# Kernel tuning notes

Hardware: AMD Instinct MI355X
Metric: run time of the kernel (lower is better)

Reference implementation:

```python
import jax, jax.numpy as jnp
from jax import lax
import numpy as np

N, I, O = 64, 8, 8
B = 512
S_EX, S_PHI, S_RHO = 10, 60, 60  # S_phi must equal S_rho (alpha loops feed S_rho-sized h into the GRUs)
N_ACTIONS, N_ROLES = 5, 7


def _gru(x, h, Wih, Whh, bih, bhh):
    # torch.nn.GRUCell math
    gi = x @ Wih.T + bih
    gh = h @ Whh.T + bhh
    ir, iz, inn = jnp.split(gi, 3, axis=-1)
    hr, hz, hn = jnp.split(gh, 3, axis=-1)
    r = jax.nn.sigmoid(ir + hr)
    zg = jax.nn.sigmoid(iz + hz)
    n = jnp.tanh(inn + r * hn)
    return (1.0 - zg) * n + zg * h


def setup_inputs() -> dict:
    key = jax.random.key(0)
    ks = jax.random.split(key, 24)
    f32 = jnp.float32
    z = jax.random.normal(ks[0], (B, N, S_EX), f32)
    dz = jax.random.normal(ks[1], (B, N, S_EX), f32)
    has = (jax.random.uniform(ks[2], (B, N)) < 0.9).astype(f32)
    adj = (jnp.triu(jax.random.uniform(ks[3], (N, N)), 1) > 0.7).astype(jnp.int32)

    def lin(k, o, i):
        return (jax.random.normal(k, (o, i), f32) * np.float32(1.0 / np.sqrt(i)))

    d = dict(z=z, dz=dz, has=has, adj=adj)
    d['Wih_f'] = lin(ks[4], 3 * S_PHI, S_RHO)
    d['Whh_f'] = lin(ks[5], 3 * S_PHI, S_PHI)
    d['bih_f'] = jax.random.normal(ks[6], (3 * S_PHI,), f32) * 0.02
    d['bhh_f'] = jax.random.normal(ks[7], (3 * S_PHI,), f32) * 0.02
    d['Wih_b'] = lin(ks[8], 3 * S_PHI, S_RHO)
    d['Whh_b'] = lin(ks[9], 3 * S_PHI, S_PHI)
    d['bih_b'] = jax.random.normal(ks[10], (3 * S_PHI,), f32) * 0.02
    d['bhh_b'] = jax.random.normal(ks[11], (3 * S_PHI,), f32) * 0.02
    d['Wf'] = lin(ks[12], S_RHO, S_PHI + 2 * S_EX)
    d['bf'] = jax.random.normal(ks[13], (S_RHO,), f32) * 0.02
    d['Wb'] = lin(ks[14], S_RHO, S_PHI + 2 * S_EX)
    d['bb'] = jax.random.normal(ks[15], (S_RHO,), f32) * 0.02
    d['Wa'] = lin(ks[16], N_ACTIONS, 2 * S_PHI)
    d['ba'] = jax.random.normal(ks[17], (N_ACTIONS,), f32) * 0.02
    d['Wc'] = lin(ks[18], 1, 2 * S_PHI)
    d['bc'] = jax.random.normal(ks[19], (1,), f32) * 0.02
    d['Wu'] = lin(ks[20], N_ROLES, 2 * S_RHO)
    d['bu'] = jax.random.normal(ks[21], (N_ROLES,), f32) * 0.02
    return d


def reference(z, dz, has, adj,
              Wih_f, Whh_f, bih_f, bhh_f,
              Wih_b, Whh_b, bih_b, bhh_b,
              Wf, bf, Wb, bb, Wa, ba, Wc, bc, Wu, bu):
    Bn, Nn = has.shape
    dt = z.dtype
    adjf = adj.astype(dt)

    # ---- forward sweep over nodes in ascending order ----
    def fwd_outer(rho, i):
        def inner(h, j):
            hn = _gru(rho[j], h, Wih_f, Whh_f, bih_f, bhh_f)
            blend = adjf[j, i] * has[:, j][:, None]  # edge exists AND source node present
            return h + blend * (hn - h), None
        h, _ = lax.scan(inner, jnp.zeros((Bn, S_PHI), dt), jnp.arange(Nn))
        rho_i = jnp.tanh(jnp.concatenate([h, z[:, i], dz[:, i]], 1) @ Wf.T + bf)
        return rho.at[i].set(rho_i), None

    rho_f, _ = lax.scan(fwd_outer, jnp.zeros((Nn, Bn, S_RHO), dt), jnp.arange(Nn))

    # ---- backward sweep over nodes in descending order ----
    def bwd_outer(rho, i):
        def inner(h, j):
            hn = _gru(rho[j], h, Wih_b, Whh_b, bih_b, bhh_b)
            blend = adjf[i, j] * has[:, j][:, None]  # out-edges of i, visited descending
            return h + blend * (hn - h), None
        h, _ = lax.scan(inner, jnp.zeros((Bn, S_PHI), dt), jnp.arange(Nn - 1, -1, -1))
        rho_i = jnp.concatenate([h, z[:, i], dz[:, i]], 1) @ Wb.T + bb
        return rho.at[i].set(rho_i), None

    rho_b, _ = lax.scan(bwd_outer, jnp.zeros((Nn, Bn, S_RHO), dt), jnp.arange(Nn - 1, -1, -1))

    # ---- aggregate outputs (last O nodes) and inputs (first I nodes) ----
    h = jnp.zeros((Bn, S_RHO), dt)
    for i in range(N - O, N):
        hn = _gru(rho_f[i], h, Wih_f, Whh_f, bih_f, bhh_f)
        h = h + has[:, i][:, None] * (hn - h)
    alpha_f = h
    h = jnp.zeros((Bn, S_RHO), dt)
    for i in reversed(range(I)):
        hn = _gru(rho_b[i], h, Wih_b, Whh_b, bih_b, bhh_b)
        h = h + has[:, i][:, None] * (hn - h)
    alpha_b = h

    ab = jnp.concatenate([alpha_f, alpha_b], 1)
    omega = ab @ Wa.T + ba          # [B, 5]
    value = ab @ Wc.T + bc          # [B, 1]

    feats = jnp.concatenate([rho_f, rho_b], -1)           # [N, B, 2*S_rho]
    psi = jnp.einsum('nbs,rs->brn', feats, Wu) + bu[None, :, None]  # [B, 7, N]
    m = has[:, None, :]
    psi = -60.0 * (1.0 - m) + psi * m  # interpolate(-60, psi, has)

    instr_prob = jax.nn.softmax(omega, axis=1)
    role_prob = jax.nn.softmax(psi, axis=2)
    return instr_prob, role_prob, value
```

## Files before the change

kernel.cpp:

```cpp
#include <hip/hip_runtime.h>
#include <hip/hip_bf16.h>

#define NN 64
#define BATCH 512
#define SP 60
#define SG 180
#define SEX 10
#define CATD 80
#define NA 5
#define NR 7
#define OO 8
#define II 8

typedef unsigned long long u64;
typedef unsigned short u16;
typedef unsigned int u32;
typedef unsigned char u8;

#define OFF_Z     0
#define OFF_DZ    327680
#define OFF_HAS   655360
#define OFF_WIHF  688128
#define OFF_WHHF  698928
#define OFF_BIHF  709728
#define OFF_BHHF  709908
#define OFF_WIHB  710088
#define OFF_WHHB  720888
#define OFF_BIHB  731688
#define OFF_BHHB  731868
#define OFF_WF    732048
#define OFF_BF    736848
#define OFF_WB    736908
#define OFF_BB    741708
#define OFF_WA    741768
#define OFF_BA    742368
#define OFF_WC    742373
#define OFF_BC    742493
#define OFF_WU    742494
#define OFF_BU    743334
#define CONV_TOTAL 743341
#define OFF_FLAG  743342
#define OFF_RHOF  743344
#define OFF_RHOB  (OFF_RHOF + 1966080)
#define OFF_ALF   (OFF_RHOB + 1966080)
#define OFF_ALB   (OFF_ALF + 30720)
#define OUT_TOTAL 232448

typedef _Float16 f16;
typedef _Float16 half2_t __attribute__((ext_vector_type(2)));
typedef _Float16 f16x8 __attribute__((ext_vector_type(8)));
typedef float f32x4 __attribute__((ext_vector_type(4)));

__device__ __forceinline__ float us2f(u16 v){
  return __uint_as_float(((u32)v) << 16);
}
__device__ __forceinline__ u16 f2bf(float f){
  __hip_bfloat16 h = __float2bfloat16(f);
  return *reinterpret_cast<u16*>(&h);
}
__device__ __forceinline__ float rcp_(float x){ return __builtin_amdgcn_rcpf(x); }
__device__ __forceinline__ float sigm(float x){
  return rcp_(1.f + __expf(-x));
}
__device__ __forceinline__ float tanh_(float x){
  float e = __expf(2.f*fabsf(x));
  float t = 1.f - 2.f*rcp_(e + 1.f);
  return copysignf(t, x);
}
__device__ __forceinline__ u32 pack2(float a, float b){
  half2_t h; h[0] = (f16)a; h[1] = (f16)b;
  return __builtin_bit_cast(u32, h);
}
__device__ __forceinline__ float fdot2_(u32 a, u32 b, float c){
  return __builtin_amdgcn_fdot2(__builtin_bit_cast(half2_t, a),
                                __builtin_bit_cast(half2_t, b), c, false);
}
__device__ __forceinline__ f16x8 bc16(uint4 v){ return __builtin_bit_cast(f16x8, v); }
__device__ __forceinline__ f32x4 mfma16(f16x8 a, f16x8 b, f32x4 c){
  return __builtin_amdgcn_mfma_f32_16x16x32_f16(a, b, c, 0, 0, 0);
}

struct HP { uint4 q[8]; };
__device__ __forceinline__ u32 hpc(const HP& p, int k){
  const uint4& v = p.q[k>>2];
  switch(k&3){ case 0: return v.x; case 1: return v.y; case 2: return v.z; default: return v.w; }
}

__device__ __forceinline__ int detect_bf16(const u32* w){
  int f = 0;
  for (int i=0;i<256;i++) f |= (w[i] == 0x3F803F80u) ? 1 : 0;
  return f;
}

__global__ __launch_bounds__(256) void conv_in(
  const void* z, const void* dz, const void* has,
  const void* WihF, const void* WhhF, const void* bihF, const void* bhhF,
  const void* WihB, const void* WhhB, const void* bihB, const void* bhhB,
  const void* Wf_, const void* bf_, const void* Wb_, const void* bb_,
  const void* Wa, const void* ba, const void* Wc, const void* bc,
  const void* Wu, const void* bu, float* ws)
{
  const int isbf = detect_bf16((const u32*)has);
  if (blockIdx.x == 0 && threadIdx.x == 0) ws[OFF_FLAG] = (float)isbf;
  int idx = blockIdx.x*256 + threadIdx.x;
  if (idx >= CONV_TOTAL) return;
  const void* src; int loc;
  if      (idx < OFF_DZ  ){ src=z;    loc=idx-OFF_Z;    }
  else if (idx < OFF_HAS ){ src=dz;   loc=idx-OFF_DZ;   }
  else if (idx < OFF_WIHF){ src=has;  loc=idx-OFF_HAS;  }
  else if (idx < OFF_WHHF){ src=WihF; loc=idx-OFF_WIHF; }
  else if (idx < OFF_BIHF){ src=WhhF; loc=idx-OFF_WHHF; }
  else if (idx < OFF_BHHF){ src=bihF; loc=idx-OFF_BIHF; }
  else if (idx < OFF_WIHB){ src=bhhF; loc=idx-OFF_BHHF; }
  else if (idx < OFF_WHHB){ src=WihB; loc=idx-OFF_WIHB; }
  else if (idx < OFF_BIHB){ src=WhhB; loc=idx-OFF_WHHB; }
  else if (idx < OFF_BHHB){ src=bihB; loc=idx-OFF_BIHB; }
  else if (idx < OFF_WF  ){ src=bhhB; loc=idx-OFF_BHHB; }
  else if (idx < OFF_BF  ){ src=Wf_;  loc=idx-OFF_WF;   }
  else if (idx < OFF_WB  ){ src=bf_;  loc=idx-OFF_BF;   }
  else if (idx < OFF_BB  ){ src=Wb_;  loc=idx-OFF_WB;   }
  else if (idx < OFF_WA  ){ src=bb_;  loc=idx-OFF_BB;   }
  else if (idx < OFF_BA  ){ src=Wa;   loc=idx-OFF_WA;   }
  else if (idx < OFF_WC  ){ src=ba;   loc=idx-OFF_BA;   }
  else if (idx < OFF_BC  ){ src=Wc;   loc=idx-OFF_WC;   }
  else if (idx < OFF_WU  ){ src=bc;   loc=idx-OFF_BC;   }
  else if (idx < OFF_BU  ){ src=Wu;   loc=idx-OFF_WU;   }
  else                    { src=bu;   loc=idx-OFF_BU;   }
  float v = isbf ? us2f(((const u16*)src)[loc]) : ((const float*)src)[loc];
  ws[idx] = v;
}

__global__ __launch_bounds__(64, 1) void dir_kernel(const int* __restrict__ adj,
                                                    float* __restrict__ ws)
{
  const int u   = threadIdx.x;
  const int ml  = u & 15;
  const int q   = u >> 4;
  const int bid = blockIdx.x;
  const int bwd = bid >> 9;
  const int b   = bid & 511;

  const float* Wih  = ws + (bwd ? OFF_WIHB : OFF_WIHF);
  const float* Whh  = ws + (bwd ? OFF_WHHB : OFF_WHHF);
  const float* bih  = ws + (bwd ? OFF_BIHB : OFF_BIHF);
  const float* bhh  = ws + (bwd ? OFF_BHHB : OFF_BHHF);
  const float* Wcat = ws + (bwd ? OFF_WB   : OFF_WF);
  const float* bcat = ws + (bwd ? OFF_BB   : OFF_BF);
  const float* zc   = ws + OFF_Z;
  const float* dzc  = ws + OFF_DZ;
  const float* hasc = ws + OFF_HAS;
  float* rho   = ws + (bwd ? OFF_RHOB : OFF_RHOF);
  float* alpha = ws + (bwd ? OFF_ALB  : OFF_ALF);

  __shared__ uint4 sH4[65][9];
  __shared__ uint4 sRhoPad[8];
  __shared__ uint4 sRhoHist[8][8];
  __shared__ float sRhoOut[NN][SP];
  __shared__ u32 sZp[NN][5];
  __shared__ u32 sDZp[NN][5];
  __shared__ float sHas[NN];
  __shared__ u64 sRowM[NN];
  __shared__ u8 sConsL[NN][64];
  __shared__ int sConsCnt[NN];

  #define ROWB(I) ((char*)&sH4[(I)][0])
  const u32 BIASW = 0x3C000000u;

  u64 rowm = 0;
  {
    for (int j=0;j<64;j++) rowm |= ((u64)(adj[u*64+j]!=0))<<j;
    sRowM[u] = rowm;
    sHas[u] = hasc[b*NN + u];
    for (int idx=u; idx<65*9; idx+=64){
      uint4 v = {0,0,0,0};
      if (idx % 9 == 7) v.w = BIASW;
      ((uint4*)sH4)[idx] = v;
    }
    if (u < 8){ uint4 v={0,0,0,0}; if (u==7) v.w = BIASW; sRhoPad[u]=v; }
    { uint4 v={0,0,0,0}; if ((u&7)==7) v.w = BIASW; ((uint4*)sRhoHist)[u]=v; }
    for (int idx=u; idx<NN*5; idx+=64){
      int n2=idx/5, p2=idx%5;
      sZp [n2][p2] = pack2(zc [(size_t)b*NN*SEX + n2*SEX + 2*p2],
                           zc [(size_t)b*NN*SEX + n2*SEX + 2*p2+1]);
      sDZp[n2][p2] = pack2(dzc[(size_t)b*NN*SEX + n2*SEX + 2*p2],
                           dzc[(size_t)b*NN*SEX + n2*SEX + 2*p2+1]);
    }
  }
  __syncthreads();
  {
    u64 cm = 0;
    if (bwd) for (int i2=0;i2<64;i2++) cm |= ((sRowM[i2]>>u)&1ULL)<<i2;
    u64 m = bwd ? cm : rowm;
    int c = 0;
    while (m){ int i2 = (int)__builtin_ctzll(m); m &= m-1; sConsL[u][c++] = (u8)i2; }
    sConsCnt[u] = c;
  }

  f16x8 Ar[4][4], Az[4][4], Anh[4][2], Ani[4][2];
  #pragma unroll
  for (int mt=0; mt<4; mt++){
    const int R = 16*mt + ml;
    const bool rok = (R < SP);
    #pragma unroll
    for (int kt=0; kt<4; kt++){
      f16x8 vr, vz;
      #pragma unroll
      for (int j=0;j<8;j++){
        const int K = 32*kt + 8*q + j;
        float wr=0.f, wz=0.f;
        if (rok){
          if (K < SP){ wr = Whh[R*SP+K]; wz = Whh[(60+R)*SP+K]; }
          else if (K >= 64 && K < 64+SP){ wr = Wih[R*SP+(K-64)]; wz = Wih[(60+R)*SP+(K-64)]; }
          else if (K == 127){ wr = bhh[R]+bih[R]; wz = bhh[60+R]+bih[60+R]; }
        }
        vr[j]=(f16)wr; vz[j]=(f16)wz;
      }
      Ar[mt][kt]=vr; Az[mt][kt]=vz;
    }
    #pragma unroll
    for (int kt=0; kt<2; kt++){
      f16x8 vn, vi;
      #pragma unroll
      for (int j=0;j<8;j++){
        const int K = 32*kt + 8*q + j;
        float wn=0.f, wi=0.f;
        if (rok){
          if (K < SP){ wn = Whh[(120+R)*SP+K]; wi = Wih[(120+R)*SP+K]; }
          else if (K == 63){ wn = bhh[120+R]; wi = bih[120+R]; }
        }
        vn[j]=(f16)wn; vi[j]=(f16)wi;
      }
      Anh[mt][kt]=vn; Ani[mt][kt]=vi;
    }
  }

  u32 wc[40];
  #pragma unroll
  for (int k=0;k<40;k++) wc[k] = pack2(Wcat[u*CATD + 2*k], Wcat[u*CATD + 2*k+1]);
  const float bct = bcat[u];
  __syncthreads();

  auto gatepass = [&](f16x8 Bh0, f16x8 Bh1, f16x8 Br0, f16x8 Br1,
                      const f32x4* Gn, int ci, bool wr, float bl){
    f32x4 Dr[4], Dz[4], Dn[4];
    #pragma unroll
    for (int mt=0;mt<4;mt++){
      f32x4 a={0,0,0,0};
      a = mfma16(Ar[mt][0], Bh0, a); a = mfma16(Ar[mt][1], Bh1, a);
      a = mfma16(Ar[mt][2], Br0, a); a = mfma16(Ar[mt][3], Br1, a);
      Dr[mt] = a;
      f32x4 c2={0,0,0,0};
      c2 = mfma16(Az[mt][0], Bh0, c2); c2 = mfma16(Az[mt][1], Bh1, c2);
      c2 = mfma16(Az[mt][2], Br0, c2); c2 = mfma16(Az[mt][3], Br1, c2);
      Dz[mt] = c2;
      f32x4 d={0,0,0,0};
      d = mfma16(Anh[mt][0], Bh0, d); d = mfma16(Anh[mt][1], Bh1, d);
      Dn[mt] = d;
    }
    #pragma unroll
    for (int mt=0;mt<4;mt++){
      char* rp = ROWB(ci) + 32*mt + 8*q;
      uint2 h2 = *(uint2*)rp;
      half2_t ha = __builtin_bit_cast(half2_t, h2.x);
      half2_t hb = __builtin_bit_cast(half2_t, h2.y);
      float hold[4] = { (float)ha[0], (float)ha[1], (float)hb[0], (float)hb[1] };
      float hw[4];
      #pragma unroll
      for (int reg=0;reg<4;reg++){
        float r_ = sigm(Dr[mt][reg]);
        float zg = sigm(Dz[mt][reg]);
        float nv = tanh_(Gn[mt][reg] + r_*Dn[mt][reg]);
        float hn_ = (1.f - zg)*nv + zg*hold[reg];
        hw[reg] = (bl != 0.f) ? hn_ : hold[reg];
      }
      if (wr && !(mt==3 && q==3)){
        uint2 o; o.x = pack2(hw[0],hw[1]); o.y = pack2(hw[2],hw[3]);
        *(uint2*)rp = o;
      }
    }
  };

  int t = bwd ? 63 : 0;
  const int dt = bwd ? -1 : 1;
  for (int s=0; s<64; s++, t+=dt){
    {
      HP ht;
      { const uint4* _r=(const uint4*)&sH4[t][0];
        #pragma unroll
        for (int _k=0;_k<8;_k++) ht.q[_k]=_r[_k]; }
      float c0 = bct, c1 = 0.f, c2 = 0.f, c3 = 0.f;
      #pragma unroll
      for (int k=0;k<28;k+=4){
        c0 = fdot2_(wc[k],   hpc(ht,k),   c0);
        c1 = fdot2_(wc[k+1], hpc(ht,k+1), c1);
        c2 = fdot2_(wc[k+2], hpc(ht,k+2), c2);
        c3 = fdot2_(wc[k+3], hpc(ht,k+3), c3);
      }
      c0 = fdot2_(wc[28], hpc(ht,28), c0);
      c1 = fdot2_(wc[29], hpc(ht,29), c1);
      #pragma unroll
      for (int p2=0;p2<5;p2++){
        c2 = fdot2_(wc[30+p2], sZp [t][p2], c2);
        c3 = fdot2_(wc[35+p2], sDZp[t][p2], c3);
      }
      float acc = (c0 + c1) + (c2 + c3);
      float rv = bwd ? acc : tanh_(acc);
      if (u < SP){
        sRhoOut[t][u] = rv;
        *(f16*)((char*)&sRhoPad[0] + 2*u) = (f16)rv;
      }
      const int slot = bwd ? t : (t - (NN-OO));
      if (slot >= 0 && slot < 8 && u < SP)
        *(f16*)((char*)&sRhoHist[slot][0] + 2*u) = (f16)rv;
    }
    __syncthreads();

    const float blendT = sHas[t];
    const int cnt = sConsCnt[t];
    if (blendT != 0.f && cnt > 0){
      const f16x8 Br0 = bc16(sRhoPad[q]);
      const f16x8 Br1 = bc16(sRhoPad[4+q]);
      f32x4 Gn[4];
      #pragma unroll
      for (int mt=0;mt<4;mt++){
        f32x4 g={0,0,0,0};
        g = mfma16(Ani[mt][0], Br0, g);
        g = mfma16(Ani[mt][1], Br1, g);
        Gn[mt] = g;
      }
      for (int p=0; 16*p < cnt; p++){
        const int idxp = 16*p + ml;
        const int ci = (idxp < cnt) ? (int)sConsL[t][idxp] : 64;
        const f16x8 Bh0 = bc16(sH4[ci][q]);
        const f16x8 Bh1 = bc16(sH4[ci][4+q]);
        gatepass(Bh0, Bh1, Br0, Br1, Gn, ci, idxp < cnt, 1.0f);
      }
    }
    __syncthreads();
  }

  for (int idx=u; idx<NN*SP; idx+=64){
    int n2 = idx/SP, s2 = idx%SP;
    rho[((size_t)n2*BATCH + b)*SP + s2] = sRhoOut[n2][s2];
  }

  for (int s2=0; s2<8; s2++){
    const int i = bwd ? (7 - s2) : (NN - OO + s2);
    const int slot = bwd ? i : (i - (NN-OO));
    const f16x8 Th0 = bc16(sH4[64][q]);
    const f16x8 Th1 = bc16(sH4[64][4+q]);
    const f16x8 Tr0 = bc16(sRhoHist[slot][q]);
    const f16x8 Tr1 = bc16(sRhoHist[slot][4+q]);
    f32x4 Gt[4];
    #pragma unroll
    for (int mt=0;mt<4;mt++){
      f32x4 g={0,0,0,0};
      g = mfma16(Ani[mt][0], Tr0, g);
      g = mfma16(Ani[mt][1], Tr1, g);
      Gt[mt] = g;
    }
    gatepass(Th0, Th1, Tr0, Tr1, Gt, 64, ml==0, sHas[i]);
    __syncthreads();
  }
  if (u < SP) alpha[(size_t)b*SP + u] = (float)*(const f16*)(ROWB(64) + 2*u);
  #undef ROWB
}

__global__ __launch_bounds__(256, 1) void head_kernel(float* __restrict__ ws,
                                                      void* __restrict__ outp)
{
  const int b = blockIdx.x;
  const int tid = threadIdx.x;
  const int isbf = (ws[OFF_FLAG] != 0.f);
  const float* hasc   = ws + OFF_HAS;
  const float* WaC    = ws + OFF_WA;
  const float* baC    = ws + OFF_BA;
  const float* WcC    = ws + OFF_WC;
  const float* bcC    = ws + OFF_BC;
  const float* WuC    = ws + OFF_WU;
  const float* buC    = ws + OFF_BU;
  const float* rhoF   = ws + OFF_RHOF;
  const float* rhoB   = ws + OFF_RHOB;
  const float* alphaF = ws + OFF_ALF;
  const float* alphaB = ws + OFF_ALB;

  __shared__ float sF[NN][121];
  __shared__ float sAB[120];
  __shared__ float sWu[NR*120];
  __shared__ float sHasR[NN];
  __shared__ float sPsi[NR][NN];
  __shared__ float sRed[NR][2];
  __shared__ float sOm[NA];

  auto wout = [&](int idx, float v){
    if (isbf) ((u16*)outp)[idx] = f2bf(v);
    else      ((float*)outp)[idx] = v;
  };

  for (int idx=tid; idx<NN*SP; idx+=256){
    int n = idx/SP, s = idx%SP;
    sF[n][s]    = rhoF[((size_t)n*BATCH + b)*SP + s];
    sF[n][60+s] = rhoB[((size_t)n*BATCH + b)*SP + s];
  }
  for (int idx=tid; idx<120; idx+=256)
    sAB[idx] = (idx<60) ? alphaF[(size_t)b*SP + idx] : alphaB[(size_t)b*SP + idx-60];
  for (int idx=tid; idx<NR*120; idx+=256) sWu[idx] = WuC[idx];
  for (int idx=tid; idx<NN; idx+=256) sHasR[idx] = hasc[b*NN + idx];
  __syncthreads();

  for (int idx=tid; idx<NR*NN; idx+=256){
    int r = idx/NN, n = idx%NN;
    float acc = buC[r];
    for (int s=0;s<120;s++) acc += sF[n][s]*sWu[r*120+s];
    sPsi[r][n] = (sHasR[n] != 0.f) ? acc : -60.f;
  }
  if (tid >= 64 && tid < 64+NA){
    int a = tid - 64;
    float acc = baC[a];
    for (int s=0;s<120;s++) acc += sAB[s]*WaC[a*120+s];
    sOm[a] = acc;
  }
  if (tid == 70){
    float acc = bcC[0];
    for (int s=0;s<120;s++) acc += sAB[s]*WcC[s];
    wout(2560 + BATCH*NR*NN + b, acc);
  }
  __syncthreads();

  if (tid < NR){
    float m = -1e30f;
    for (int n=0;n<NN;n++) m = fmaxf(m, sPsi[tid][n]);
    float ssum = 0.f;
    for (int n=0;n<NN;n++) ssum += __expf(sPsi[tid][n]-m);
    sRed[tid][0] = m; sRed[tid][1] = 1.f/ssum;
  }
  if (tid == 8){
    float m = -1e30f;
    for (int a=0;a<NA;a++) m = fmaxf(m, sOm[a]);
    float e[NA]; float ssum = 0.f;
    for (int a=0;a<NA;a++){ e[a] = __expf(sOm[a]-m); ssum += e[a]; }
    for (int a=0;a<NA;a++) wout(b*NA + a, e[a]/ssum);
  }
  __syncthreads();

  for (int idx=tid; idx<NR*NN; idx+=256){
    int r = idx/NN, n = idx%NN;
    float v = __expf(sPsi[r][n]-sRed[r][0]) * sRed[r][1];
    wout(2560 + (size_t)b*NR*NN + idx, v);
  }
}

extern "C" void kernel_launch(void* const* d_in, const int* in_sizes, int n_in,
                              void* d_out, int out_size, void* d_ws, size_t ws_size,
                              hipStream_t stream)
{
  const int* adj = (const int*)d_in[3];
  float* ws = (float*)d_ws;

  conv_in<<<(CONV_TOTAL+255)/256, 256, 0, stream>>>(
      d_in[0], d_in[1], d_in[2],
      d_in[4], d_in[5], d_in[6], d_in[7],
      d_in[8], d_in[9], d_in[10], d_in[11],
      d_in[12], d_in[13], d_in[14], d_in[15],
      d_in[16], d_in[17], d_in[18], d_in[19],
      d_in[20], d_in[21], ws);

  dir_kernel<<<1024, 64, 0, stream>>>(adj, ws);

  head_kernel<<<512, 256, 0, stream>>>(ws, d_out);
}
```

Baseline: 302.1 us.

## Split GRU gate row tiles across two wavefronts per block in dir_kernel

Each dir_kernel block now runs two wavefronts instead of one. Each wavefront owns two of the four 16-row M tiles of the GRU gate matrices, which halves per-thread weight registers and the MFMA work per wave on the serial node recurrence. The rho projection still runs on wave 0 only. Extra __syncthreads are added so the read of hidden state happens before either wave writes it back. This adds more barriers inside the sequential loop, and wave 1 sits idle during the rho step.

```diff
diff --git a/kernel.cpp b/kernel.cpp
--- a/kernel.cpp
+++ b/kernel.cpp
@@ -130,10 +130,12 @@
   ws[idx] = v;
 }
 
-__global__ __launch_bounds__(64, 1) void dir_kernel(const int* __restrict__ adj,
-                                                    float* __restrict__ ws)
+__global__ __launch_bounds__(128, 2) void dir_kernel(const int* __restrict__ adj,
+                                                     float* __restrict__ ws)
 {
-  const int u   = threadIdx.x;
+  const int tid = threadIdx.x;
+  const int w   = tid >> 6;
+  const int u   = tid & 63;
   const int ml  = u & 15;
   const int q   = u >> 4;
   const int bid = blockIdx.x;
@@ -166,19 +168,21 @@
   #define ROWB(I) ((char*)&sH4[(I)][0])
   const u32 BIASW = 0x3C000000u;
 
-  u64 rowm = 0;
   {
-    for (int j=0;j<64;j++) rowm |= ((u64)(adj[u*64+j]!=0))<<j;
-    sRowM[u] = rowm;
-    sHas[u] = hasc[b*NN + u];
-    for (int idx=u; idx<65*9; idx+=64){
+    if (tid < 64){
+      u64 rowm = 0;
+      for (int j=0;j<64;j++) rowm |= ((u64)(adj[tid*64+j]!=0))<<j;
+      sRowM[tid] = rowm;
+      sHas[tid] = hasc[b*NN + tid];
+    }
+    for (int idx=tid; idx<65*9; idx+=128){
       uint4 v = {0,0,0,0};
       if (idx % 9 == 7) v.w = BIASW;
       ((uint4*)sH4)[idx] = v;
     }
-    if (u < 8){ uint4 v={0,0,0,0}; if (u==7) v.w = BIASW; sRhoPad[u]=v; }
-    { uint4 v={0,0,0,0}; if ((u&7)==7) v.w = BIASW; ((uint4*)sRhoHist)[u]=v; }
-    for (int idx=u; idx<NN*5; idx+=64){
+    if (tid < 8){ uint4 v={0,0,0,0}; if (tid==7) v.w = BIASW; sRhoPad[tid]=v; }
+    if (tid < 64){ uint4 v={0,0,0,0}; if ((tid&7)==7) v.w = BIASW; ((uint4*)sRhoHist)[tid]=v; }
+    for (int idx=tid; idx<NN*5; idx+=128){
       int n2=idx/5, p2=idx%5;
       sZp [n2][p2] = pack2(zc [(size_t)b*NN*SEX + n2*SEX + 2*p2],
                            zc [(size_t)b*NN*SEX + n2*SEX + 2*p2+1]);
@@ -187,18 +191,19 @@
     }
   }
   __syncthreads();
-  {
+  if (tid < 64){
     u64 cm = 0;
-    if (bwd) for (int i2=0;i2<64;i2++) cm |= ((sRowM[i2]>>u)&1ULL)<<i2;
-    u64 m = bwd ? cm : rowm;
+    if (bwd) for (int i2=0;i2<64;i2++) cm |= ((sRowM[i2]>>tid)&1ULL)<<i2;
+    u64 m = bwd ? cm : sRowM[tid];
     int c = 0;
-    while (m){ int i2 = (int)__builtin_ctzll(m); m &= m-1; sConsL[u][c++] = (u8)i2; }
-    sConsCnt[u] = c;
-  }
-
-  f16x8 Ar[4][4], Az[4][4], Anh[4][2], Ani[4][2];
+    while (m){ int i2 = (int)__builtin_ctzll(m); m &= m-1; sConsL[tid][c++] = (u8)i2; }
+    sConsCnt[tid] = c;
+  }
+
+  f16x8 Ar[2][4], Az[2][4], Anh[2][2], Ani[2][2];
   #pragma unroll
-  for (int mt=0; mt<4; mt++){
+  for (int mtl=0; mtl<2; mtl++){
+    const int mt = 2*w + mtl;
     const int R = 16*mt + ml;
     const bool rok = (R < SP);
     #pragma unroll
@@ -215,7 +220,7 @@
         }
         vr[j]=(f16)wr; vz[j]=(f16)wz;
       }
-      Ar[mt][kt]=vr; Az[mt][kt]=vz;
+      Ar[mtl][kt]=vr; Az[mtl][kt]=vz;
     }
     #pragma unroll
     for (int kt=0; kt<2; kt++){
@@ -230,35 +235,39 @@
         }
         vn[j]=(f16)wn; vi[j]=(f16)wi;
       }
-      Anh[mt][kt]=vn; Ani[mt][kt]=vi;
+      Anh[mtl][kt]=vn; Ani[mtl][kt]=vi;
     }
   }
 
   u32 wc[40];
-  #pragma unroll
-  for (int k=0;k<40;k++) wc[k] = pack2(Wcat[u*CATD + 2*k], Wcat[u*CATD + 2*k+1]);
-  const float bct = bcat[u];
+  float bct = 0.f;
+  if (w == 0){
+    #pragma unroll
+    for (int k=0;k<40;k++) wc[k] = pack2(Wcat[u*CATD + 2*k], Wcat[u*CATD + 2*k+1]);
+    bct = bcat[u];
+  }
   __syncthreads();
 
   auto gatepass = [&](f16x8 Bh0, f16x8 Bh1, f16x8 Br0, f16x8 Br1,
                       const f32x4* Gn, int ci, bool wr, float bl){
-    f32x4 Dr[4], Dz[4], Dn[4];
-    #pragma unroll
-    for (int mt=0;mt<4;mt++){
+    f32x4 Dr[2], Dz[2], Dn[2];
+    #pragma unroll
+    for (int mtl=0;mtl<2;mtl++){
       f32x4 a={0,0,0,0};
-      a = mfma16(Ar[mt][0], Bh0, a); a = mfma16(Ar[mt][1], Bh1, a);
-      a = mfma16(Ar[mt][2], Br0, a); a = mfma16(Ar[mt][3], Br1, a);
-      Dr[mt] = a;
+      a = mfma16(Ar[mtl][0], Bh0, a); a = mfma16(Ar[mtl][1], Bh1, a);
+      a = mfma16(Ar[mtl][2], Br0, a); a = mfma16(Ar[mtl][3], Br1, a);
+      Dr[mtl] = a;
       f32x4 c2={0,0,0,0};
-      c2 = mfma16(Az[mt][0], Bh0, c2); c2 = mfma16(Az[mt][1], Bh1, c2);
-      c2 = mfma16(Az[mt][2], Br0, c2); c2 = mfma16(Az[mt][3], Br1, c2);
-      Dz[mt] = c2;
+      c2 = mfma16(Az[mtl][0], Bh0, c2); c2 = mfma16(Az[mtl][1], Bh1, c2);
+      c2 = mfma16(Az[mtl][2], Br0, c2); c2 = mfma16(Az[mtl][3], Br1, c2);
+      Dz[mtl] = c2;
       f32x4 d={0,0,0,0};
-      d = mfma16(Anh[mt][0], Bh0, d); d = mfma16(Anh[mt][1], Bh1, d);
-      Dn[mt] = d;
-    }
-    #pragma unroll
-    for (int mt=0;mt<4;mt++){
+      d = mfma16(Anh[mtl][0], Bh0, d); d = mfma16(Anh[mtl][1], Bh1, d);
+      Dn[mtl] = d;
+    }
+    #pragma unroll
+    for (int mtl=0;mtl<2;mtl++){
+      const int mt = 2*w + mtl;
       char* rp = ROWB(ci) + 32*mt + 8*q;
       uint2 h2 = *(uint2*)rp;
       half2_t ha = __builtin_bit_cast(half2_t, h2.x);
@@ -267,9 +276,9 @@
       float hw[4];
       #pragma unroll
       for (int reg=0;reg<4;reg++){
-        float r_ = sigm(Dr[mt][reg]);
-        float zg = sigm(Dz[mt][reg]);
-        float nv = tanh_(Gn[mt][reg] + r_*Dn[mt][reg]);
+        float r_ = sigm(Dr[mtl][reg]);
+        float zg = sigm(Dz[mtl][reg]);
+        float nv = tanh_(Gn[mtl][reg] + r_*Dn[mtl][reg]);
         float hn_ = (1.f - zg)*nv + zg*hold[reg];
         hw[reg] = (bl != 0.f) ? hn_ : hold[reg];
       }
@@ -283,7 +292,7 @@
   int t = bwd ? 63 : 0;
   const int dt = bwd ? -1 : 1;
   for (int s=0; s<64; s++, t+=dt){
-    {
+    if (w == 0){
       HP ht;
       { const uint4* _r=(const uint4*)&sH4[t][0];
         #pragma unroll
@@ -320,26 +329,28 @@
     if (blendT != 0.f && cnt > 0){
       const f16x8 Br0 = bc16(sRhoPad[q]);
       const f16x8 Br1 = bc16(sRhoPad[4+q]);
-      f32x4 Gn[4];
-      #pragma unroll
-      for (int mt=0;mt<4;mt++){
+      f32x4 Gn[2];
+      #pragma unroll
+      for (int mtl=0;mtl<2;mtl++){
         f32x4 g={0,0,0,0};
-        g = mfma16(Ani[mt][0], Br0, g);
-        g = mfma16(Ani[mt][1], Br1, g);
-        Gn[mt] = g;
-      }
-      for (int p=0; 16*p < cnt; p++){
+        g = mfma16(Ani[mtl][0], Br0, g);
+        g = mfma16(Ani[mtl][1], Br1, g);
+        Gn[mtl] = g;
+      }
+      const int np = (cnt + 15) >> 4;
+      for (int p=0; p<np; p++){
         const int idxp = 16*p + ml;
         const int ci = (idxp < cnt) ? (int)sConsL[t][idxp] : 64;
         const f16x8 Bh0 = bc16(sH4[ci][q]);
         const f16x8 Bh1 = bc16(sH4[ci][4+q]);
+        __syncthreads();
         gatepass(Bh0, Bh1, Br0, Br1, Gn, ci, idxp < cnt, 1.0f);
       }
     }
     __syncthreads();
   }
 
-  for (int idx=u; idx<NN*SP; idx+=64){
+  for (int idx=tid; idx<NN*SP; idx+=128){
     int n2 = idx/SP, s2 = idx%SP;
     rho[((size_t)n2*BATCH + b)*SP + s2] = sRhoOut[n2][s2];
   }
@@ -351,18 +362,19 @@
     const f16x8 Th1 = bc16(sH4[64][4+q]);
     const f16x8 Tr0 = bc16(sRhoHist[slot][q]);
     const f16x8 Tr1 = bc16(sRhoHist[slot][4+q]);
-    f32x4 Gt[4];
-    #pragma unroll
-    for (int mt=0;mt<4;mt++){
+    f32x4 Gt[2];
+    #pragma unroll
+    for (int mtl=0;mtl<2;mtl++){
       f32x4 g={0,0,0,0};
-      g = mfma16(Ani[mt][0], Tr0, g);
-      g = mfma16(Ani[mt][1], Tr1, g);
-      Gt[mt] = g;
-    }
+      g = mfma16(Ani[mtl][0], Tr0, g);
+      g = mfma16(Ani[mtl][1], Tr1, g);
+      Gt[mtl] = g;
+    }
+    __syncthreads();
     gatepass(Th0, Th1, Tr0, Tr1, Gt, 64, ml==0, sHas[i]);
     __syncthreads();
   }
-  if (u < SP) alpha[(size_t)b*SP + u] = (float)*(const f16*)(ROWB(64) + 2*u);
+  if (tid < SP) alpha[(size_t)b*SP + tid] = (float)*(const f16*)(ROWB(64) + 2*tid);
   #undef ROWB
 }
 
@@ -465,7 +477,7 @@
       d_in[16], d_in[17], d_in[18], d_in[19],
       d_in[20], d_in[21], ws);
 
-  dir_kernel<<<1024, 64, 0, stream>>>(adj, ws);
+  dir_kernel<<<1024, 128, 0, stream>>>(adj, ws);
 
   head_kernel<<<512, 256, 0, stream>>>(ws, d_out);
 }
```

Measured after the change: 274.3 us. 1.1x faster.
